# Kernel tuning notes

Hardware: AMD Instinct MI355X
Metric: run time of the kernel (lower is better)

The kernel has to match this reference:

```python
import jax, jax.numpy as jnp
import numpy as np

N = 131072  # nodes
E = 4096    # edges (unused by forward)
MID = 32    # multiplicity of irreps_mid = 32x0e + 32x1o
NF = 128    # multiplicity of node_feat_irreps = 128x0e + 128x1o
INV_SQRT3 = 0.5773502691896258          # |w3j(1,1,0)| = |w3j(0,1,1)| = 1/sqrt(3)
PW_QQ_S = (1.0 / 2048.0) ** 0.5         # path weight: alpha = dim(0e)/ (32*32 + 32*32)
PW_QQ_V = (3.0 / 2048.0) ** 0.5         # path weight: alpha = dim(1o)/ (32*32 + 32*32)
PW_DOWN = (1.0 / 8192.0) ** 0.5         # path weight: alpha = dim(0e)/ (32*128 + 32*128)


def setup_inputs() -> dict:
    key = jax.random.key(0)
    ks = jax.random.split(key, 20)
    inp = {
        "node_feats": jax.random.normal(ks[0], (N, NF + 3 * NF), jnp.float32),
        "charges_0": jax.random.normal(ks[1], (N, 4), jnp.float32),
        "charges_induced": jax.random.normal(ks[2], (N, 4), jnp.float32),
        "edge_feats": jax.random.normal(ks[3], (E, 8), jnp.float32),
        "edge_attrs": jax.random.normal(ks[4], (E, 9), jnp.float32),
        "field_feats": jax.random.normal(ks[5], (N, 4), jnp.float32),
        "edge_index": jax.random.randint(ks[6], (2, E), 0, N, dtype=jnp.int32),
        "batch": jnp.sort(jax.random.randint(ks[7], (N,), 0, 64, dtype=jnp.int32)),
        # o3.Linear(1x0e+1x1o -> 32x0e+32x1o) params (fan_in = 1 per path -> norm 1)
        "Wa_s": jax.random.normal(ks[8], (1, MID), jnp.float32),
        "Wa_v": jax.random.normal(ks[9], (1, MID), jnp.float32),
        "b_a": jnp.zeros((MID,), jnp.float32),
        "Wb_s": jax.random.normal(ks[10], (1, MID), jnp.float32),
        "Wb_v": jax.random.normal(ks[11], (1, MID), jnp.float32),
        "b_b": jnp.zeros((MID,), jnp.float32),
        # FullyConnectedTensorProduct(mid, mid -> mid) uvw weights, one per CG path
        "W_ss": jax.random.normal(ks[12], (MID, MID, MID), jnp.float32),  # 0e x 0e -> 0e
        "W_vv": jax.random.normal(ks[13], (MID, MID, MID), jnp.float32),  # 1o x 1o -> 0e
        "W_sv": jax.random.normal(ks[14], (MID, MID, MID), jnp.float32),  # 0e x 1o -> 1o
        "W_vs": jax.random.normal(ks[15], (MID, MID, MID), jnp.float32),  # 1o x 0e -> 1o
        # FullyConnectedTensorProduct(mid, node_feats -> 1x0e) uvw weights
        "Wd_s": jax.random.normal(ks[16], (MID, NF), jnp.float32),        # 0e x 0e -> 0e
        "Wd_v": jax.random.normal(ks[17], (MID, NF), jnp.float32),        # 1o x 1o -> 0e
    }
    return inp


def reference(node_feats, charges_0, charges_induced, edge_feats, edge_attrs,
              field_feats, edge_index, batch,
              Wa_s, Wa_v, b_a, Wb_s, Wb_v, b_b,
              W_ss, W_vv, W_sv, W_vs, Wd_s, Wd_v):
    # split irreps blocks
    s0, v0 = charges_0[:, :1], charges_0[:, 1:4]            # [N,1], [N,3]
    si, vi = charges_induced[:, :1], charges_induced[:, 1:4]
    nf_s = node_feats[:, :NF]                               # [N,128]
    nf_v = node_feats[:, NF:].reshape(-1, NF, 3)            # [N,128,3]

    # charges = linear_qa(charges_induced) + linear_qb(charges_0)  (bias only on 0e)
    s = si @ Wa_s + b_a + s0 @ Wb_s + b_b                   # [N,32]
    v = (jnp.einsum('nui,uw->nwi', vi[:, None, :], Wa_v)
         + jnp.einsum('nui,uw->nwi', v0[:, None, :], Wb_v))  # [N,32,3]

    # qq = FullyConnectedTensorProduct(charges, charges) -> 32x0e + 32x1o
    qs = PW_QQ_S * (jnp.einsum('nu,nv,uvw->nw', s, s, W_ss)
                    + INV_SQRT3 * jnp.einsum('nui,nvi,uvw->nw', v, v, W_vv))      # [N,32]
    qv = (PW_QQ_V * INV_SQRT3) * (jnp.einsum('nu,nvi,uvw->nwi', s, v, W_sv)
                                  + jnp.einsum('nui,nv,uvw->nwi', v, s, W_vs))    # [N,32,3]

    # energy = FullyConnectedTensorProduct(qq, node_feats) -> 1x0e, then squeeze
    energy = PW_DOWN * (jnp.einsum('nu,nv,uv->n', qs, nf_s, Wd_s)
                        + INV_SQRT3 * jnp.einsum('nui,nvi,uv->n', qv, nf_v, Wd_v))  # [N]
    return energy
```

## Files before the change

### kernel.cpp

```cpp
#include <hip/hip_runtime.h>


#define TBLK 128
#define NNODES 131072

typedef __attribute__((address_space(1))) const void gas_void;
typedef __attribute__((address_space(3))) void las_void;
__device__ __forceinline__ void gl_lds16(const void* g, void* l) {
  __builtin_amdgcn_global_load_lds((gas_void*)g, (las_void*)l, 16, 0, 0);
}

__global__ void precompute_coeff(
    const float* __restrict__ Wa_s, const float* __restrict__ Wa_v,
    const float* __restrict__ b_a,  const float* __restrict__ Wb_s,
    const float* __restrict__ Wb_v, const float* __restrict__ b_b,
    const float* __restrict__ W_ss, const float* __restrict__ W_vv,
    const float* __restrict__ W_sv, const float* __restrict__ W_vs,
    float* __restrict__ partial)
{
  __shared__ float As[32], Bs[32], Cc[32], Avv[32], Bvv[32];
  __shared__ float red[8][480];
  const int t = threadIdx.x;
  if (t < 32) {
    As[t] = Wa_s[t]; Bs[t] = Wb_s[t]; Cc[t] = b_a[t] + b_b[t];
    Avv[t] = Wa_v[t]; Bvv[t] = Wb_v[t];
  }
  __syncthreads();
  const int w = t & 31;
  const int grp = t >> 5;
  const int chunk = blockIdx.x * 8 + grp;
  float acc[15];
  #pragma unroll
  for (int k = 0; k < 15; ++k) acc[k] = 0.f;
  #pragma unroll
  for (int j = 0; j < 4; ++j) {
    const int p = chunk * 4 + j;
    const int u = p >> 5, v = p & 31;
    const float wss = W_ss[p * 32 + w];
    const float wvv = W_vv[p * 32 + w];
    const float wsv = W_sv[p * 32 + w];
    const float wvs = W_vs[p * 32 + w];
    const float au = As[u], bu = Bs[u], cu = Cc[u], pu = Avv[u], qu = Bvv[u];
    const float av = As[v], bv = Bs[v], cv = Cc[v], pv = Avv[v], qv = Bvv[v];
    acc[0]  = fmaf(au * av, wss, acc[0]);
    acc[1]  = fmaf(au * bv + bu * av, wss, acc[1]);
    acc[2]  = fmaf(bu * bv, wss, acc[2]);
    acc[3]  = fmaf(au * cv + cu * av, wss, acc[3]);
    acc[4]  = fmaf(bu * cv + cu * bv, wss, acc[4]);
    acc[5]  = fmaf(cu * cv, wss, acc[5]);
    acc[6]  = fmaf(pu * pv, wvv, acc[6]);
    acc[7]  = fmaf(pu * qv + qu * pv, wvv, acc[7]);
    acc[8]  = fmaf(qu * qv, wvv, acc[8]);
    acc[9]  = fmaf(au * pv, wsv, fmaf(pu * av, wvs, acc[9]));
    acc[10] = fmaf(au * qv, wsv, fmaf(qu * av, wvs, acc[10]));
    acc[11] = fmaf(bu * pv, wsv, fmaf(pu * bv, wvs, acc[11]));
    acc[12] = fmaf(bu * qv, wsv, fmaf(qu * bv, wvs, acc[12]));
    acc[13] = fmaf(cu * pv, wsv, fmaf(pu * cv, wvs, acc[13]));
    acc[14] = fmaf(cu * qv, wsv, fmaf(qu * cv, wvs, acc[14]));
  }
  #pragma unroll
  for (int k = 0; k < 15; ++k) red[grp][k * 32 + w] = acc[k];
  __syncthreads();
  for (int kk = grp; kk < 15; kk += 8) {
    float s = 0.f;
    #pragma unroll
    for (int b = 0; b < 8; ++b) s += red[b][kk * 32 + w];
    partial[blockIdx.x * 480 + kk * 32 + w] = s;
  }
}

__global__ void precompute_M(
    const float* __restrict__ Wd_s, const float* __restrict__ Wd_v,
    const float* __restrict__ partial,
    float* __restrict__ Ms, float* __restrict__ Mv)
{
  __shared__ float cf[480];
  const int t = threadIdx.x;
  if (t < 480) {
    float s = 0.f;
    for (int b = 0; b < 32; ++b) s += partial[b * 480 + t];
    cf[t] = s;
  }
  __syncthreads();
  if (t < 128) {
    const int f = t;
    float as[9], av[6];
    #pragma unroll
    for (int k = 0; k < 9; ++k) as[k] = 0.f;
    #pragma unroll
    for (int k = 0; k < 6; ++k) av[k] = 0.f;
    for (int w = 0; w < 32; ++w) {
      const float wds = Wd_s[w * 128 + f];
      const float wdv = Wd_v[w * 128 + f];
      #pragma unroll
      for (int k = 0; k < 9; ++k) as[k] = fmaf(cf[k * 32 + w], wds, as[k]);
      #pragma unroll
      for (int k = 0; k < 6; ++k) av[k] = fmaf(cf[(9 + k) * 32 + w], wdv, av[k]);
    }
    const float sP = 1.0f / 4096.0f;
    const float sQ = 0.57735026918962576451f / 4096.0f;
    #pragma unroll
    for (int k = 0; k < 6; ++k) Ms[f * 16 + k] = as[k] * sP;
    #pragma unroll
    for (int k = 0; k < 3; ++k) Ms[f * 16 + 6 + k] = as[6 + k] * sQ;
    #pragma unroll
    for (int k = 0; k < 6; ++k) Mv[f * 8 + k] = av[k] * sQ;
  }
}

__device__ __forceinline__ float wcomb9(const float* __restrict__ p,
    float m0, float m1, float m2, float a, float b,
    float m6, float m7, float m8)
{
  float r = p[5];
  r = fmaf(m0, p[0], r);
  r = fmaf(m1, p[1], r);
  r = fmaf(m2, p[2], r);
  r = fmaf(a,  p[3], r);
  r = fmaf(b,  p[4], r);
  r = fmaf(m6, p[6], r);
  r = fmaf(m7, p[7], r);
  r = fmaf(m8, p[8], r);
  return r;
}

__device__ __forceinline__ void stage_tile(
    const float* __restrict__ nf, float4* __restrict__ buf,
    int node0, int tl, int t)
{
  const int wv   = t >> 6;
  const int lane = t & 63;
  const int r_in = lane >> 3;
  const int s_in = lane & 7;
  #pragma unroll
  for (int q = 0; q < 8; ++q) {
    const int p   = wv * 8 + q;
    const int row = p * 8 + r_in;
    const int gs  = s_in ^ (r_in & 7);
    const float4* g = reinterpret_cast<const float4*>(nf)
                    + ((size_t)(node0 + row) * 128 + tl * 8 + gs);
    gl_lds16(g, buf + p * 64);
  }
}

template<int PHASE>
__device__ __forceinline__ void vtile(
    const float4* __restrict__ cur, int t, int fb,
    const float* __restrict__ Mv,
    float g0, float g1, float g2, float d0, float d1, float d2,
    float& P, float& Q,
    float& SP0, float& SP2, float& SP4,
    float& SQ1, float& SQ3, float& SQ5)
{
  const int sw = t & 7;
  #pragma unroll
  for (int j = 0; j < 8; ++j) {
    const float4 x = cur[t * 8 + (j ^ sw)];
    const float xs[4] = {x.x, x.y, x.z, x.w};
    #pragma unroll
    for (int e = 0; e < 4; ++e) {
      const int l = 4 * j + e;
      const int i = (PHASE + l) % 3;
      const float gg = (i == 0) ? g0 : ((i == 1) ? g1 : g2);
      const float dd = (i == 0) ? d0 : ((i == 1) ? d1 : d2);
      P = fmaf(gg, xs[e], P);
      Q = fmaf(dd, xs[e], Q);
      if (i == 2) {
        const float* cv = Mv + (fb + (PHASE + l) / 3) * 8;
        SP0 = fmaf(cv[0], P, SP0);
        SQ1 = fmaf(cv[1], Q, SQ1);
        SP2 = fmaf(cv[2], P, SP2);
        SQ3 = fmaf(cv[3], Q, SQ3);
        SP4 = fmaf(cv[4], P, SP4);
        SQ5 = fmaf(cv[5], Q, SQ5);
        P = 0.f; Q = 0.f;
      }
    }
  }
}

__global__ __launch_bounds__(TBLK, 2) void energy_main(
    const float* __restrict__ nf,
    const float* __restrict__ ch0,
    const float* __restrict__ chi,
    const float* __restrict__ Ms,
    const float* __restrict__ Mv,
    float* __restrict__ out)
{
  __shared__ float4 buf[2][1024];
  const int t = threadIdx.x;
  const int node0 = blockIdx.x * TBLK;

  const float4 cc0 = reinterpret_cast<const float4*>(ch0)[node0 + t];
  const float4 cci = reinterpret_cast<const float4*>(chi)[node0 + t];

  stage_tile(nf, &buf[0][0], node0, 0, t);

  const float alpha = cci.x, g0 = cci.y, g1 = cci.z, g2 = cci.w;
  const float beta  = cc0.x, d0 = cc0.y, d1 = cc0.z, d2 = cc0.w;
  const float m0 = alpha * alpha, m1 = alpha * beta, m2 = beta * beta;
  const float m6 = fmaf(g0, g0, fmaf(g1, g1, g2 * g2));
  const float m7 = fmaf(g0, d0, fmaf(g1, d1, g2 * d2));
  const float m8 = fmaf(d0, d0, fmaf(d1, d1, d2 * d2));

  const int sw = t & 7;
  float es0 = 0.f, es1 = 0.f, es2 = 0.f, es3 = 0.f;
  float P = 0.f, Q = 0.f;
  float SP0 = 0.f, SP2 = 0.f, SP4 = 0.f, SQ1 = 0.f, SQ3 = 0.f, SQ5 = 0.f;

  #pragma unroll
  for (int tl = 0; tl < 16; ++tl) {
    __builtin_amdgcn_s_waitcnt(0);
    __syncthreads();
    if (tl < 15) stage_tile(nf, &buf[(tl + 1) & 1][0], node0, tl + 1, t);
    const float4* cur = &buf[tl & 1][0];

    if (tl < 4) {
      const float* cp0 = Ms + tl * 32 * 16;
      #pragma unroll
      for (int j = 0; j < 8; ++j) {
        const float4 x = cur[t * 8 + (j ^ sw)];
        const float* cp = cp0 + j * 64;
        es0 = fmaf(x.x, wcomb9(cp,      m0, m1, m2, alpha, beta, m6, m7, m8), es0);
        es1 = fmaf(x.y, wcomb9(cp + 16, m0, m1, m2, alpha, beta, m6, m7, m8), es1);
        es2 = fmaf(x.z, wcomb9(cp + 32, m0, m1, m2, alpha, beta, m6, m7, m8), es2);
        es3 = fmaf(x.w, wcomb9(cp + 48, m0, m1, m2, alpha, beta, m6, m7, m8), es3);
      }
    } else {
      const int k  = tl - 4;
      const int cb = 32 * k;
      const int fb = cb / 3;
      switch (cb % 3) {
        case 0:  vtile<0>(cur, t, fb, Mv, g0, g1, g2, d0, d1, d2, P, Q, SP0, SP2, SP4, SQ1, SQ3, SQ5); break;
        case 1:  vtile<1>(cur, t, fb, Mv, g0, g1, g2, d0, d1, d2, P, Q, SP0, SP2, SP4, SQ1, SQ3, SQ5); break;
        default: vtile<2>(cur, t, fb, Mv, g0, g1, g2, d0, d1, d2, P, Q, SP0, SP2, SP4, SQ1, SQ3, SQ5); break;
      }
    }
  }

  const float ev = fmaf(alpha, SP0 + SQ1, fmaf(beta, SP2 + SQ3, SP4 + SQ5));
  out[node0 + t] = (es0 + es1) + (es2 + es3) + ev;
}

extern "C" void kernel_launch(void* const* d_in, const int* in_sizes, int n_in,
                              void* d_out, int out_size, void* d_ws, size_t ws_size,
                              hipStream_t stream)
{
  const float* node_feats      = (const float*)d_in[0];
  const float* charges_0       = (const float*)d_in[1];
  const float* charges_induced = (const float*)d_in[2];
  const float* Wa_s = (const float*)d_in[8];
  const float* Wa_v = (const float*)d_in[9];
  const float* b_a  = (const float*)d_in[10];
  const float* Wb_s = (const float*)d_in[11];
  const float* Wb_v = (const float*)d_in[12];
  const float* b_b  = (const float*)d_in[13];
  const float* W_ss = (const float*)d_in[14];
  const float* W_vv = (const float*)d_in[15];
  const float* W_sv = (const float*)d_in[16];
  const float* W_vs = (const float*)d_in[17];
  const float* Wd_s = (const float*)d_in[18];
  const float* Wd_v = (const float*)d_in[19];

  float* ws      = (float*)d_ws;
  float* Ms      = ws;
  float* Mv      = ws + 2048;
  float* partial = ws + 3072;

  precompute_coeff<<<32, 256, 0, stream>>>(Wa_s, Wa_v, b_a, Wb_s, Wb_v, b_b,
                                           W_ss, W_vv, W_sv, W_vs, partial);
  precompute_M<<<1, 512, 0, stream>>>(Wd_s, Wd_v, partial, Ms, Mv);
  energy_main<<<NNODES / TBLK, TBLK, 0, stream>>>(node_feats, charges_0,
                                                  charges_induced, Ms, Mv,
                                                  (float*)d_out);
}
```

Measured before the change: 435.0 us.

## Map 32 lanes per node with register-resident coefficients and shuffle reduction

Replaces the one-thread-per-node design, which staged feature tiles through LDS with double buffering, with one node per 32 lanes. Each lane reads contiguous float4 slices of the node row directly from global memory, so loads are coalesced. The per-feature coefficient matrices Ms and Mv now sit in registers, loaded once per thread. The partial energies are combined with a xor-shuffle reduction and lane 0 writes the result. This removes the LDS staging, barriers and per-node scalar loads of the coefficients, at the cost of some redundant charge-coefficient arithmetic per lane and shuffle overhead.

```diff
diff --git a/kernel.cpp b/kernel.cpp
--- a/kernel.cpp
+++ b/kernel.cpp
@@ -1,14 +1,11 @@
 #include <hip/hip_runtime.h>
 
 
-#define TBLK 128
 #define NNODES 131072
-
-typedef __attribute__((address_space(1))) const void gas_void;
-typedef __attribute__((address_space(3))) void las_void;
-__device__ __forceinline__ void gl_lds16(const void* g, void* l) {
-  __builtin_amdgcn_global_load_lds((gas_void*)g, (las_void*)l, 16, 0, 0);
-}
+#define TBLK 256
+#define NODES_PER_PASS 8
+#define PASSES 8
+#define NPB (NODES_PER_PASS * PASSES)
 
 __global__ void precompute_coeff(
     const float* __restrict__ Wa_s, const float* __restrict__ Wa_v,
@@ -108,78 +105,7 @@
   }
 }
 
-__device__ __forceinline__ float wcomb9(const float* __restrict__ p,
-    float m0, float m1, float m2, float a, float b,
-    float m6, float m7, float m8)
-{
-  float r = p[5];
-  r = fmaf(m0, p[0], r);
-  r = fmaf(m1, p[1], r);
-  r = fmaf(m2, p[2], r);
-  r = fmaf(a,  p[3], r);
-  r = fmaf(b,  p[4], r);
-  r = fmaf(m6, p[6], r);
-  r = fmaf(m7, p[7], r);
-  r = fmaf(m8, p[8], r);
-  return r;
-}
-
-__device__ __forceinline__ void stage_tile(
-    const float* __restrict__ nf, float4* __restrict__ buf,
-    int node0, int tl, int t)
-{
-  const int wv   = t >> 6;
-  const int lane = t & 63;
-  const int r_in = lane >> 3;
-  const int s_in = lane & 7;
-  #pragma unroll
-  for (int q = 0; q < 8; ++q) {
-    const int p   = wv * 8 + q;
-    const int row = p * 8 + r_in;
-    const int gs  = s_in ^ (r_in & 7);
-    const float4* g = reinterpret_cast<const float4*>(nf)
-                    + ((size_t)(node0 + row) * 128 + tl * 8 + gs);
-    gl_lds16(g, buf + p * 64);
-  }
-}
-
-template<int PHASE>
-__device__ __forceinline__ void vtile(
-    const float4* __restrict__ cur, int t, int fb,
-    const float* __restrict__ Mv,
-    float g0, float g1, float g2, float d0, float d1, float d2,
-    float& P, float& Q,
-    float& SP0, float& SP2, float& SP4,
-    float& SQ1, float& SQ3, float& SQ5)
-{
-  const int sw = t & 7;
-  #pragma unroll
-  for (int j = 0; j < 8; ++j) {
-    const float4 x = cur[t * 8 + (j ^ sw)];
-    const float xs[4] = {x.x, x.y, x.z, x.w};
-    #pragma unroll
-    for (int e = 0; e < 4; ++e) {
-      const int l = 4 * j + e;
-      const int i = (PHASE + l) % 3;
-      const float gg = (i == 0) ? g0 : ((i == 1) ? g1 : g2);
-      const float dd = (i == 0) ? d0 : ((i == 1) ? d1 : d2);
-      P = fmaf(gg, xs[e], P);
-      Q = fmaf(dd, xs[e], Q);
-      if (i == 2) {
-        const float* cv = Mv + (fb + (PHASE + l) / 3) * 8;
-        SP0 = fmaf(cv[0], P, SP0);
-        SQ1 = fmaf(cv[1], Q, SQ1);
-        SP2 = fmaf(cv[2], P, SP2);
-        SQ3 = fmaf(cv[3], Q, SQ3);
-        SP4 = fmaf(cv[4], P, SP4);
-        SQ5 = fmaf(cv[5], Q, SQ5);
-        P = 0.f; Q = 0.f;
-      }
-    }
-  }
-}
-
-__global__ __launch_bounds__(TBLK, 2) void energy_main(
+__global__ __launch_bounds__(TBLK) void energy_main(
     const float* __restrict__ nf,
     const float* __restrict__ ch0,
     const float* __restrict__ chi,
@@ -187,59 +113,100 @@
     const float* __restrict__ Mv,
     float* __restrict__ out)
 {
-  __shared__ float4 buf[2][1024];
-  const int t = threadIdx.x;
-  const int node0 = blockIdx.x * TBLK;
-
-  const float4 cc0 = reinterpret_cast<const float4*>(ch0)[node0 + t];
-  const float4 cci = reinterpret_cast<const float4*>(chi)[node0 + t];
-
-  stage_tile(nf, &buf[0][0], node0, 0, t);
-
-  const float alpha = cci.x, g0 = cci.y, g1 = cci.z, g2 = cci.w;
-  const float beta  = cc0.x, d0 = cc0.y, d1 = cc0.z, d2 = cc0.w;
-  const float m0 = alpha * alpha, m1 = alpha * beta, m2 = beta * beta;
-  const float m6 = fmaf(g0, g0, fmaf(g1, g1, g2 * g2));
-  const float m7 = fmaf(g0, d0, fmaf(g1, d1, g2 * d2));
-  const float m8 = fmaf(d0, d0, fmaf(d1, d1, d2 * d2));
-
-  const int sw = t & 7;
-  float es0 = 0.f, es1 = 0.f, es2 = 0.f, es3 = 0.f;
-  float P = 0.f, Q = 0.f;
-  float SP0 = 0.f, SP2 = 0.f, SP4 = 0.f, SQ1 = 0.f, SQ3 = 0.f, SQ5 = 0.f;
-
-  #pragma unroll
-  for (int tl = 0; tl < 16; ++tl) {
-    __builtin_amdgcn_s_waitcnt(0);
-    __syncthreads();
-    if (tl < 15) stage_tile(nf, &buf[(tl + 1) & 1][0], node0, tl + 1, t);
-    const float4* cur = &buf[tl & 1][0];
-
-    if (tl < 4) {
-      const float* cp0 = Ms + tl * 32 * 16;
-      #pragma unroll
-      for (int j = 0; j < 8; ++j) {
-        const float4 x = cur[t * 8 + (j ^ sw)];
-        const float* cp = cp0 + j * 64;
-        es0 = fmaf(x.x, wcomb9(cp,      m0, m1, m2, alpha, beta, m6, m7, m8), es0);
-        es1 = fmaf(x.y, wcomb9(cp + 16, m0, m1, m2, alpha, beta, m6, m7, m8), es1);
-        es2 = fmaf(x.z, wcomb9(cp + 32, m0, m1, m2, alpha, beta, m6, m7, m8), es2);
-        es3 = fmaf(x.w, wcomb9(cp + 48, m0, m1, m2, alpha, beta, m6, m7, m8), es3);
+  const int t    = threadIdx.x;
+  const int s32  = t & 31;
+  const int gidx = t >> 5;
+
+  float ms[4][9];
+  float mv[4][6];
+  {
+    const float4* Ms4 = reinterpret_cast<const float4*>(Ms);
+    const float4* Mv4 = reinterpret_cast<const float4*>(Mv);
+    #pragma unroll
+    for (int fl = 0; fl < 4; ++fl) {
+      const int f = 4 * s32 + fl;
+      const float4 a = Ms4[f * 4 + 0];
+      const float4 b = Ms4[f * 4 + 1];
+      const float4 c = Ms4[f * 4 + 2];
+      ms[fl][0] = a.x; ms[fl][1] = a.y; ms[fl][2] = a.z; ms[fl][3] = a.w;
+      ms[fl][4] = b.x; ms[fl][5] = b.y; ms[fl][6] = b.z; ms[fl][7] = b.w;
+      ms[fl][8] = c.x;
+      const float4 u = Mv4[f * 2 + 0];
+      const float4 v = Mv4[f * 2 + 1];
+      mv[fl][0] = u.x; mv[fl][1] = u.y; mv[fl][2] = u.z; mv[fl][3] = u.w;
+      mv[fl][4] = v.x; mv[fl][5] = v.y;
+    }
+  }
+
+  const float4* nf4 = reinterpret_cast<const float4*>(nf);
+  const float4* c04 = reinterpret_cast<const float4*>(ch0);
+  const float4* ci4 = reinterpret_cast<const float4*>(chi);
+
+  const int node0 = blockIdx.x * NPB;
+
+  #pragma unroll 2
+  for (int p = 0; p < PASSES; ++p) {
+    const int node  = node0 + p * NODES_PER_PASS + gidx;
+    const size_t rb = (size_t)node * 128;
+
+    const float4 cc0 = c04[node];
+    const float4 cci = ci4[node];
+    const float4 xs  = nf4[rb + s32];
+    const float4 xv0 = nf4[rb + 32 + 3 * s32 + 0];
+    const float4 xv1 = nf4[rb + 32 + 3 * s32 + 1];
+    const float4 xv2 = nf4[rb + 32 + 3 * s32 + 2];
+
+    const float alpha = cci.x, g0 = cci.y, g1 = cci.z, g2 = cci.w;
+    const float beta  = cc0.x, d0 = cc0.y, d1 = cc0.z, d2 = cc0.w;
+    const float m0 = alpha * alpha, m1 = alpha * beta, m2 = beta * beta;
+    const float m6 = fmaf(g0, g0, fmaf(g1, g1, g2 * g2));
+    const float m7 = fmaf(g0, d0, fmaf(g1, d1, g2 * d2));
+    const float m8 = fmaf(d0, d0, fmaf(d1, d1, d2 * d2));
+
+    float e = 0.f;
+
+    const float xse[4] = {xs.x, xs.y, xs.z, xs.w};
+    #pragma unroll
+    for (int fl = 0; fl < 4; ++fl) {
+      float r = ms[fl][5];
+      r = fmaf(m0,    ms[fl][0], r);
+      r = fmaf(m1,    ms[fl][1], r);
+      r = fmaf(m2,    ms[fl][2], r);
+      r = fmaf(alpha, ms[fl][3], r);
+      r = fmaf(beta,  ms[fl][4], r);
+      r = fmaf(m6,    ms[fl][6], r);
+      r = fmaf(m7,    ms[fl][7], r);
+      r = fmaf(m8,    ms[fl][8], r);
+      e = fmaf(xse[fl], r, e);
+    }
+
+    const float xve[12] = {xv0.x, xv0.y, xv0.z, xv0.w,
+                           xv1.x, xv1.y, xv1.z, xv1.w,
+                           xv2.x, xv2.y, xv2.z, xv2.w};
+    const float gg[3] = {g0, g1, g2};
+    const float dd[3] = {d0, d1, d2};
+    float P = 0.f, Q = 0.f;
+    #pragma unroll
+    for (int q = 0; q < 12; ++q) {
+      const int i = q % 3;
+      P = fmaf(gg[i], xve[q], P);
+      Q = fmaf(dd[i], xve[q], Q);
+      if (i == 2) {
+        const int fl = q / 3;
+        const float wP = fmaf(alpha, mv[fl][0], fmaf(beta, mv[fl][2], mv[fl][4]));
+        const float wQ = fmaf(alpha, mv[fl][1], fmaf(beta, mv[fl][3], mv[fl][5]));
+        e = fmaf(P, wP, fmaf(Q, wQ, e));
+        P = 0.f; Q = 0.f;
       }
-    } else {
-      const int k  = tl - 4;
-      const int cb = 32 * k;
-      const int fb = cb / 3;
-      switch (cb % 3) {
-        case 0:  vtile<0>(cur, t, fb, Mv, g0, g1, g2, d0, d1, d2, P, Q, SP0, SP2, SP4, SQ1, SQ3, SQ5); break;
-        case 1:  vtile<1>(cur, t, fb, Mv, g0, g1, g2, d0, d1, d2, P, Q, SP0, SP2, SP4, SQ1, SQ3, SQ5); break;
-        default: vtile<2>(cur, t, fb, Mv, g0, g1, g2, d0, d1, d2, P, Q, SP0, SP2, SP4, SQ1, SQ3, SQ5); break;
-      }
-    }
-  }
-
-  const float ev = fmaf(alpha, SP0 + SQ1, fmaf(beta, SP2 + SQ3, SP4 + SQ5));
-  out[node0 + t] = (es0 + es1) + (es2 + es3) + ev;
+    }
+
+    e += __shfl_xor(e, 1);
+    e += __shfl_xor(e, 2);
+    e += __shfl_xor(e, 4);
+    e += __shfl_xor(e, 8);
+    e += __shfl_xor(e, 16);
+    if (s32 == 0) out[node] = e;
+  }
 }
 
 extern "C" void kernel_launch(void* const* d_in, const int* in_sizes, int n_in,
@@ -270,7 +237,7 @@
   precompute_coeff<<<32, 256, 0, stream>>>(Wa_s, Wa_v, b_a, Wb_s, Wb_v, b_b,
                                            W_ss, W_vv, W_sv, W_vs, partial);
   precompute_M<<<1, 512, 0, stream>>>(Wd_s, Wd_v, partial, Ms, Mv);
-  energy_main<<<NNODES / TBLK, TBLK, 0, stream>>>(node_feats, charges_0,
-                                                  charges_induced, Ms, Mv,
-                                                  (float*)d_out);
-}
+  energy_main<<<NNODES / NPB, TBLK, 0, stream>>>(node_feats, charges_0,
+                                                 charges_induced, Ms, Mv,
+                                                 (float*)d_out);
+}
```

Measured after the change: 412.8 us. 1.05x faster.
